# Optimization experiments

Measured on AMD Instinct MI355X. Metric: run time of the kernel, lower is better.

## Reference

```python
import jax, jax.numpy as jnp
import numpy as np

HEADS = 16
DIM_HEAD = 64


def setup_inputs() -> dict:
    key = jax.random.key(0)
    k1, k2, k3, k4 = jax.random.split(key, 4)
    B, T, D = 4, 1024, 1024
    x = jax.random.normal(k1, (B, T, D), dtype=jnp.float32)
    w_qkv = jax.random.normal(k2, (3 * HEADS * DIM_HEAD, D), dtype=jnp.float32) * (1.0 / np.sqrt(D))
    w_out = jax.random.normal(k3, (D, HEADS * DIM_HEAD), dtype=jnp.float32) * (1.0 / np.sqrt(HEADS * DIM_HEAD))
    rel_bias = jax.random.normal(k4, (2 * 1024 - 1, HEADS), dtype=jnp.float32) * 0.02
    return {"x": x, "w_qkv": w_qkv, "w_out": w_out, "rel_bias": rel_bias}


def reference(x, w_qkv, w_out, rel_bias):
    b, t, _ = x.shape
    h, dh = HEADS, DIM_HEAD
    scale = dh ** (-0.5)
    qkv = x @ w_qkv.T  # [b, t, 3*h*dh]
    # einops 'b t (d k h) -> k b h t d': last axis factors as (dh, 3, h)
    qkv = qkv.reshape(b, t, dh, 3, h).transpose(3, 0, 4, 1, 2)  # [3, b, h, t, dh]
    q, k, v = qkv[0], qkv[1], qkv[2]
    scores = jnp.einsum('bhid,bhjd->bhij', q, k) * scale  # [b, h, t, t]
    # relative position bias: rel[i,j] = j - i + t - 1
    rel = jnp.arange(t)[None, :] - jnp.arange(t)[:, None] + (t - 1)  # [t, t]
    bias = rel_bias[rel]  # [t, t, h]
    scores = scores + bias.transpose(2, 0, 1)[None]  # [b, h, t, t]
    attn = jax.nn.softmax(scores, axis=-1)
    out = jnp.einsum('bhij,bhjd->bhid', attn, v)  # [b, h, t, dh]
    out = out.transpose(0, 2, 1, 3).reshape(b, t, h * dh)  # 'b h t d -> b t (h d)'
    return out @ w_out.T
```

## Files before the change

### kernel.cpp

```cpp
#include <hip/hip_runtime.h>
#include <hip/hip_bf16.h>

typedef short bf16x8 __attribute__((ext_vector_type(8)));
typedef float f32x4  __attribute__((ext_vector_type(4)));

typedef __attribute__((address_space(3))) void lds_t;
typedef __attribute__((address_space(1))) void gbl_t;

#define MFMA16(a,b,c) __builtin_amdgcn_mfma_f32_16x16x32_bf16((a),(b),(c),0,0,0)

__device__ __forceinline__ unsigned short f2bf(float f) {
    __hip_bfloat16 h = __float2bfloat16(f);
    return __builtin_bit_cast(unsigned short, h);
}
__device__ __forceinline__ float bf2f(unsigned short u) {
    __hip_bfloat16 h = __builtin_bit_cast(__hip_bfloat16, u);
    return __bfloat162float(h);
}

__global__ void prep_all(const float* __restrict__ x,
                         const float* __restrict__ w_qkv,
                         const float* __restrict__ w_out,
                         unsigned short* __restrict__ A1h,
                         unsigned short* __restrict__ W1h,
                         unsigned short* __restrict__ W3h) {
    const int NX = 4096 * 256, NW1 = 3072 * 256, NW3 = 1024 * 256;
    for (int idx = blockIdx.x * blockDim.x + threadIdx.x; idx < NX + NW1 + NW3;
         idx += gridDim.x * blockDim.x) {
        if (idx < NX) {
            int base = idx * 4;
            float4 v = *reinterpret_cast<const float4*>(x + base);
            ushort4 hi;
            hi.x = f2bf(v.x); hi.y = f2bf(v.y);
            hi.z = f2bf(v.z); hi.w = f2bf(v.w);
            *reinterpret_cast<ushort4*>(A1h + base) = hi;
        } else if (idx < NX + NW1) {
            int base = (idx - NX) * 4;
            int n = base >> 10, c = base & 1023;
            int d = n & 63, which = n >> 10, h = (n >> 6) & 15;
            int srow = d * 48 + which * 16 + h;
            float4 v =
                *reinterpret_cast<const float4*>(w_qkv + (size_t)srow * 1024 + c);
            ushort4 hi;
            hi.x = f2bf(v.x); hi.y = f2bf(v.y);
            hi.z = f2bf(v.z); hi.w = f2bf(v.w);
            *reinterpret_cast<ushort4*>(W1h + (size_t)n * 1024 + c) = hi;
        } else {
            int base = (idx - NX - NW1) * 4;
            float4 v = *reinterpret_cast<const float4*>(w_out + base);
            ushort4 hi;
            hi.x = f2bf(v.x); hi.y = f2bf(v.y);
            hi.z = f2bf(v.z); hi.w = f2bf(v.w);
            *reinterpret_cast<ushort4*>(W3h + base) = hi;
        }
    }
}

__global__ __launch_bounds__(512, 1) void gemm256_hi(
    const unsigned short* __restrict__ A, const unsigned short* __restrict__ B,
    unsigned short* __restrict__ outQ, unsigned short* __restrict__ outK,
    unsigned short* __restrict__ outV) {
    __shared__ unsigned short lds[65536];
    const int tid = threadIdx.x;
    const int wid = tid >> 6, lane = tid & 63;
    const int lrow = lane & 15, lgrp = lane >> 4;
    const int wr = wid >> 2, wc = wid & 3;
    const int mtile = blockIdx.y * 256, ntile = blockIdx.x * 256;

    const int csw0 = (lgrp ^ (lrow & 7)) * 8;
    const int csw1 = ((4 | lgrp) ^ (lrow & 7)) * 8;
    const int arowb = (wr * 128 + lrow) * 64;
    const int browb = (wc * 64 + lrow) * 64;

    const int srow = tid >> 3;
    const int schunk = tid & 7;
    const int gchunk = schunk ^ (srow & 7);
    const unsigned short* Abase = A + (size_t)(mtile + srow) * 1024 + gchunk * 8;
    const unsigned short* Bbase = B + (size_t)(ntile + srow) * 1024 + gchunk * 8;
    const int sdst = srow * 64 + schunk * 8;

    f32x4 acc[8][4];
#pragma unroll
    for (int i = 0; i < 8; ++i)
#pragma unroll
        for (int j = 0; j < 4; ++j) {
            f32x4 z = {0.f, 0.f, 0.f, 0.f};
            acc[i][j] = z;
        }

#pragma unroll
    for (int e = 0; e < 4; ++e)
        __builtin_amdgcn_global_load_lds(
            (const gbl_t*)(Abase + (size_t)e * 64 * 1024),
            (lds_t*)(lds + e * 4096 + sdst), 16, 0, 0);
#pragma unroll
    for (int e = 0; e < 4; ++e)
        __builtin_amdgcn_global_load_lds(
            (const gbl_t*)(Bbase + (size_t)e * 64 * 1024),
            (lds_t*)(lds + 32768 + e * 4096 + sdst), 16, 0, 0);
    asm volatile("s_waitcnt vmcnt(0)" ::: "memory");
    __syncthreads();

    for (int s = 0; s < 16; ++s) {
        const int cur = s & 1;
        const unsigned short* abuf = lds + cur * 16384;
        const unsigned short* bbuf = lds + 32768 + cur * 16384;
        const int nx = cur ^ 1;
        const int kb = (s + 1) * 64;

        if (s < 15) {
#pragma unroll
            for (int e = 0; e < 4; ++e)
                __builtin_amdgcn_global_load_lds(
                    (const gbl_t*)(Abase + (size_t)e * 64 * 1024 + kb),
                    (lds_t*)(lds + nx * 16384 + e * 4096 + sdst), 16, 0, 0);
        }
        {
            bf16x8 af[8], bfv[4];
#pragma unroll
            for (int i = 0; i < 8; ++i)
                af[i] = *reinterpret_cast<const bf16x8*>(abuf + arowb + i * 1024 +
                                                         csw0);
#pragma unroll
            for (int j = 0; j < 4; ++j)
                bfv[j] = *reinterpret_cast<const bf16x8*>(bbuf + browb +
                                                          j * 1024 + csw0);
            __builtin_amdgcn_s_setprio(1);
#pragma unroll
            for (int i = 0; i < 8; ++i)
#pragma unroll
                for (int j = 0; j < 4; ++j)
                    acc[i][j] = MFMA16(af[i], bfv[j], acc[i][j]);
            __builtin_amdgcn_s_setprio(0);
        }
        if (s < 15) {
#pragma unroll
            for (int e = 0; e < 4; ++e)
                __builtin_amdgcn_global_load_lds(
                    (const gbl_t*)(Bbase + (size_t)e * 64 * 1024 + kb),
                    (lds_t*)(lds + 32768 + nx * 16384 + e * 4096 + sdst), 16, 0,
                    0);
        }
        {
            bf16x8 af[8], bfv[4];
#pragma unroll
            for (int i = 0; i < 8; ++i)
                af[i] = *reinterpret_cast<const bf16x8*>(abuf + arowb + i * 1024 +
                                                         csw1);
#pragma unroll
            for (int j = 0; j < 4; ++j)
                bfv[j] = *reinterpret_cast<const bf16x8*>(bbuf + browb +
                                                          j * 1024 + csw1);
            __builtin_amdgcn_s_setprio(1);
#pragma unroll
            for (int i = 0; i < 8; ++i)
#pragma unroll
                for (int j = 0; j < 4; ++j)
                    acc[i][j] = MFMA16(af[i], bfv[j], acc[i][j]);
            __builtin_amdgcn_s_setprio(0);
        }

        if (s < 15) {
            asm volatile("s_waitcnt vmcnt(0)" ::: "memory");
            __syncthreads();
        }
    }

#pragma unroll
    for (int i = 0; i < 8; ++i) {
#pragma unroll
        for (int j = 0; j < 4; ++j) {
#pragma unroll
            for (int r = 0; r < 4; ++r) {
                float v = acc[i][j][r];
                int m = mtile + wr * 128 + i * 16 + lgrp * 4 + r;
                int n = ntile + wc * 64 + j * 16 + lrow;
                int which = n >> 10;
                int hh = (n >> 6) & 15;
                int d = n & 63;
                int b = m >> 10, t = m & 1023;
                unsigned short* dstp =
                    (which == 0) ? outQ : ((which == 1) ? outK : outV);
                dstp[((size_t)((b << 4) + hh) * 1024 + t) * 64 + d] = f2bf(v);
            }
        }
    }
}

__global__ __launch_bounds__(256, 3) void gemm_out_v5(
    const unsigned short* __restrict__ A, const unsigned short* __restrict__ B,
    float* __restrict__ outF) {
    __shared__ unsigned short As[2][64 * 64];
    __shared__ unsigned short Bs[2][128 * 64];
    const int tid = threadIdx.x;
    const int wid = tid >> 6, lane = tid & 63;
    const int lrow = lane & 15, lgrp = lane >> 4;
    const int wr = wid >> 1, wc = wid & 1;
    const int h = blockIdx.x;
    const int xcd = h & 7, within = h >> 3;
    const int mtile = (xcd * 8 + (within & 7)) * 64;
    const int ntile = (within >> 3) * 128;

    const int srow = tid >> 3;
    const int schunk = (tid & 7) ^ (srow & 7);
    const unsigned short* Abase = A + (size_t)(mtile + srow) * 1024 + schunk * 8;
    const unsigned short* Bbase = B + (size_t)(ntile + srow) * 1024 + schunk * 8;

    const int csw0 = (lgrp ^ (lrow & 7)) * 8;
    const int csw1 = ((4 | lgrp) ^ (lrow & 7)) * 8;
    const int arow = wr * 32 + lrow;
    const int brow = wc * 64 + lrow;

    f32x4 acc[2][4];
#pragma unroll
    for (int i = 0; i < 2; ++i)
#pragma unroll
        for (int j = 0; j < 4; ++j) {
            f32x4 z = {0.f, 0.f, 0.f, 0.f};
            acc[i][j] = z;
        }

#pragma unroll
    for (int e = 0; e < 2; ++e)
        __builtin_amdgcn_global_load_lds(
            (const gbl_t*)(Abase + (size_t)e * 32 * 1024),
            (lds_t*)(&As[0][0] + e * 2048 + tid * 8), 16, 0, 0);
#pragma unroll
    for (int e = 0; e < 4; ++e)
        __builtin_amdgcn_global_load_lds(
            (const gbl_t*)(Bbase + (size_t)e * 32 * 1024),
            (lds_t*)(&Bs[0][0] + e * 2048 + tid * 8), 16, 0, 0);
    asm volatile("s_waitcnt vmcnt(0)" ::: "memory");
    __syncthreads();

    for (int s = 0; s < 16; ++s) {
        const int cur = s & 1;
        if (s < 15) {
            const int kb = (s + 1) * 64;
            const int nx = cur ^ 1;
#pragma unroll
            for (int e = 0; e < 2; ++e)
                __builtin_amdgcn_global_load_lds(
                    (const gbl_t*)(Abase + (size_t)e * 32 * 1024 + kb),
                    (lds_t*)(&As[nx][0] + e * 2048 + tid * 8), 16, 0, 0);
#pragma unroll
            for (int e = 0; e < 4; ++e)
                __builtin_amdgcn_global_load_lds(
                    (const gbl_t*)(Bbase + (size_t)e * 32 * 1024 + kb),
                    (lds_t*)(&Bs[nx][0] + e * 2048 + tid * 8), 16, 0, 0);
        }
        bf16x8 a0[2], a1[2], b0[4], b1[4];
#pragma unroll
        for (int i = 0; i < 2; ++i) {
            a0[i] = *reinterpret_cast<const bf16x8*>(&As[cur][0] +
                                                     (arow + i * 16) * 64 + csw0);
            a1[i] = *reinterpret_cast<const bf16x8*>(&As[cur][0] +
                                                     (arow + i * 16) * 64 + csw1);
        }
#pragma unroll
        for (int j = 0; j < 4; ++j) {
            b0[j] = *reinterpret_cast<const bf16x8*>(&Bs[cur][0] +
                                                     (brow + j * 16) * 64 + csw0);
            b1[j] = *reinterpret_cast<const bf16x8*>(&Bs[cur][0] +
                                                     (brow + j * 16) * 64 + csw1);
        }
        __builtin_amdgcn_s_setprio(1);
#pragma unroll
        for (int i = 0; i < 2; ++i)
#pragma unroll
            for (int j = 0; j < 4; ++j) {
                acc[i][j] = MFMA16(a0[i], b0[j], acc[i][j]);
                acc[i][j] = MFMA16(a1[i], b1[j], acc[i][j]);
            }
        __builtin_amdgcn_s_setprio(0);
        if (s < 15) {
            asm volatile("s_waitcnt vmcnt(0)" ::: "memory");
            __syncthreads();
        }
    }

#pragma unroll
    for (int i = 0; i < 2; ++i)
#pragma unroll
        for (int j = 0; j < 4; ++j)
#pragma unroll
            for (int r = 0; r < 4; ++r) {
                int m = mtile + wr * 32 + i * 16 + lgrp * 4 + r;
                int n = ntile + wc * 64 + j * 16 + lrow;
                outF[(size_t)m * 1024 + n] = acc[i][j][r];
            }
}

__global__ __launch_bounds__(256) void transpose_v(
    const unsigned short* __restrict__ Vb, unsigned short* __restrict__ Vtg) {
    __shared__ unsigned short L[64][72];
    const int tt = blockIdx.x, bh = blockIdx.y;
    const int tid = threadIdx.x;
#pragma unroll
    for (int e = 0; e < 2; ++e) {
        int chunk = e * 256 + tid;
        int r = chunk >> 3, c = (chunk & 7) * 8;
        uint4 v = *reinterpret_cast<const uint4*>(
            Vb + ((size_t)bh * 1024 + tt * 64 + r) * 64 + c);
        *reinterpret_cast<uint4*>(&L[r][c]) = v;
    }
    __syncthreads();
#pragma unroll
    for (int e = 0; e < 2; ++e) {
        int chunk = e * 256 + tid;
        int d = chunk >> 3, t0 = (chunk & 7) * 8;
        unsigned short tmp[8];
#pragma unroll
        for (int u = 0; u < 8; ++u) tmp[u] = L[t0 + u][d];
        *reinterpret_cast<uint4*>(Vtg + ((size_t)bh * 64 + d) * 1024 + tt * 64 +
                                  t0) = *reinterpret_cast<const uint4*>(tmp);
    }
}

__global__ __launch_bounds__(512) void attn_kernel(
    const unsigned short* __restrict__ Qb, const unsigned short* __restrict__ Kb,
    const unsigned short* __restrict__ Vtg, const float* __restrict__ rel_bias,
    unsigned short* __restrict__ A3) {
    const int bh = blockIdx.x;
    const int qt = blockIdx.y;
    const int b = bh >> 4, h = bh & 15;
    const int tid = threadIdx.x;
    const int w = tid >> 6, lane = tid & 63;
    const int lrow = lane & 15, lgrp = lane >> 4;
    const float LOG2E = 1.4426950408889634f;
    const float SCALE2 = 0.125f * 1.4426950408889634f;
    const float THR = 11.5f;

    __shared__ unsigned short Ks[2][64 * 64];
    __shared__ unsigned short Vs[2][64 * 64];
    __shared__ unsigned short Ps[8][16 * 64];
    __shared__ float BiasF[1152];

    const unsigned short* Ktile = Kb + (size_t)bh * 1024 * 64;
    const unsigned short* Vtile = Vtg + (size_t)bh * 64 * 1024;

    const unsigned short* Qp =
        Qb + ((size_t)bh * 1024 + qt * 128 + w * 16 + lrow) * 64;
    bf16x8 qa0 = *reinterpret_cast<const bf16x8*>(Qp + lgrp * 8);
    bf16x8 qa1 = *reinterpret_cast<const bf16x8*>(Qp + 32 + lgrp * 8);

    const int sr0 = w * 8 + (lane >> 3);
    const int sc_lo = lane & 7;

    float m_run = -3.0e38f;
    float l_run = 0.f;
    f32x4 o_acc[4];
#pragma unroll
    for (int n = 0; n < 4; n++) {
        f32x4 z = {0.f, 0.f, 0.f, 0.f};
        o_acc[n] = z;
    }

    const int bbase = lgrp * 4 + 127 - w * 16 - lrow;

    {
        {
            int r = sr0;
            int c = sc_lo ^ (r & 7);
            __builtin_amdgcn_global_load_lds(
                (const gbl_t*)(Ktile + (size_t)r * 64 + c * 8),
                (lds_t*)(&Ks[0][0] + w * 512), 16, 0, 0);
            __builtin_amdgcn_global_load_lds(
                (const gbl_t*)(Vtile + (size_t)r * 1024 + c * 8),
                (lds_t*)(&Vs[0][0] + w * 512), 16, 0, 0);
        }
        const int rbase = 896 - qt * 128;
        for (int t = tid; t < 1151; t += 512)
            BiasF[t] = rel_bias[(size_t)(t + rbase) * 16 + h] * LOG2E;
        asm volatile("s_waitcnt vmcnt(0)" ::: "memory");
        __syncthreads();
    }

    for (int kv = 0; kv < 16; ++kv) {
        const int cur = kv & 1;
        const int j0 = kv * 64;
        if (kv < 15) {
            const int j0n = (kv + 1) * 64;
            int r = sr0;
            int c = sc_lo ^ (r & 7);
            __builtin_amdgcn_global_load_lds(
                (const gbl_t*)(Ktile + (size_t)(j0n + r) * 64 + c * 8),
                (lds_t*)(&Ks[cur ^ 1][0] + w * 512), 16, 0, 0);
            __builtin_amdgcn_global_load_lds(
                (const gbl_t*)(Vtile + (size_t)r * 1024 + j0n + c * 8),
                (lds_t*)(&Vs[cur ^ 1][0] + w * 512), 16, 0, 0);
        }

        const unsigned short* kbuf = &Ks[cur][0];
        f32x4 s[4];
        __builtin_amdgcn_s_setprio(1);
#pragma unroll
        for (int f = 0; f < 4; ++f) {
            int krow = f * 16 + lrow;
            int sw0 = (lgrp ^ (lrow & 7)) * 8;
            int sw1 = ((4 | lgrp) ^ (lrow & 7)) * 8;
            bf16x8 kb0 = *reinterpret_cast<const bf16x8*>(kbuf + krow * 64 + sw0);
            bf16x8 kb1 = *reinterpret_cast<const bf16x8*>(kbuf + krow * 64 + sw1);
            f32x4 z = {0.f, 0.f, 0.f, 0.f};
            z = MFMA16(kb0, qa0, z);
            z = MFMA16(kb1, qa1, z);
            s[f] = z;
        }
        __builtin_amdgcn_s_setprio(0);

        float x[4][4];
        float pm = -3.0e38f;
#pragma unroll
        for (int f = 0; f < 4; ++f)
#pragma unroll
            for (int r = 0; r < 4; ++r) {
                float xv = s[f][r] * SCALE2 + BiasF[j0 + bbase + f * 16 + r];
                x[f][r] = xv;
                pm = fmaxf(pm, xv);
            }
        pm = fmaxf(pm, __shfl_xor(pm, 16));
        pm = fmaxf(pm, __shfl_xor(pm, 32));

        if (!__all(pm - m_run <= THR)) {
            float mnew = fmaxf(m_run, pm);
            float corr = __builtin_amdgcn_exp2f(m_run - mnew);
            m_run = mnew;
            l_run *= corr;
            float cb[4];
#pragma unroll
            for (int r = 0; r < 4; ++r) cb[r] = __shfl(corr, lgrp * 4 + r);
#pragma unroll
            for (int n = 0; n < 4; n++)
#pragma unroll
                for (int r = 0; r < 4; r++) o_acc[n][r] *= cb[r];
        }

        float su = 0.f;
#pragma unroll
        for (int f = 0; f < 4; ++f)
#pragma unroll
            for (int r = 0; r < 4; ++r) {
                float pv = __builtin_amdgcn_exp2f(x[f][r] - m_run);
                x[f][r] = pv;
                su += pv;
            }
        l_run += su;

#pragma unroll
        for (int f = 0; f < 4; ++f) {
            unsigned int plo, phi;
            asm("v_cvt_pk_bf16_f32 %0, %1, %2"
                : "=v"(plo)
                : "v"(x[f][0]), "v"(x[f][1]));
            asm("v_cvt_pk_bf16_f32 %0, %1, %2"
                : "=v"(phi)
                : "v"(x[f][2]), "v"(x[f][3]));
            const int chunk = (f * 2 + (lgrp >> 1)) ^ (lrow & 7);
            uint2 pw;
            pw.x = plo;
            pw.y = phi;
            *reinterpret_cast<uint2*>(
                &Ps[w][lrow * 64 + chunk * 8 + (lgrp & 1) * 4]) = pw;
        }

        const unsigned short* vbuf = &Vs[cur][0];
        __builtin_amdgcn_s_setprio(1);
#pragma unroll
        for (int jc = 0; jc < 2; ++jc) {
            int pc = ((4 * jc + lgrp) ^ (lrow & 7)) * 8;
            bf16x8 pa =
                *reinterpret_cast<const bf16x8*>(&Ps[w][0] + lrow * 64 + pc);
#pragma unroll
            for (int n = 0; n < 4; n++) {
                int vrow = n * 16 + lrow;
                bf16x8 vb =
                    *reinterpret_cast<const bf16x8*>(vbuf + vrow * 64 + pc);
                o_acc[n] = MFMA16(pa, vb, o_acc[n]);
            }
        }
        __builtin_amdgcn_s_setprio(0);

        if (kv < 15) {
            asm volatile("s_waitcnt vmcnt(0)" ::: "memory");
            __syncthreads();
        }
    }

    float lt = l_run + __shfl_xor(l_run, 16);
    lt += __shfl_xor(lt, 32);
    float rl[4];
#pragma unroll
    for (int r = 0; r < 4; ++r) rl[r] = 1.0f / __shfl(lt, lgrp * 4 + r);

#pragma unroll
    for (int n = 0; n < 4; n++) {
#pragma unroll
        for (int r = 0; r < 4; r++) {
            float val = o_acc[n][r] * rl[r];
            int ia = qt * 128 + w * 16 + lgrp * 4 + r;
            size_t m = (size_t)b * 1024 + ia;
            int col = h * 64 + n * 16 + lrow;
            A3[m * 1024 + col] = f2bf(val);
        }
    }
}

extern "C" void kernel_launch(void* const* d_in, const int* in_sizes, int n_in,
                              void* d_out, int out_size, void* d_ws,
                              size_t ws_size, hipStream_t stream) {
    const float* x = (const float*)d_in[0];
    const float* w_qkv = (const float*)d_in[1];
    const float* w_out = (const float*)d_in[2];
    const float* rel_bias = (const float*)d_in[3];
    float* out = (float*)d_out;

    char* ws = (char*)d_ws;
    size_t off = 0;
    auto alloc = [&](size_t bytes) {
        char* p = ws + off;
        off += (bytes + 255) & ~(size_t)255;
        return p;
    };
    unsigned short* A1h = (unsigned short*)alloc((size_t)4096 * 1024 * 2);
    unsigned short* W1h = (unsigned short*)alloc((size_t)3072 * 1024 * 2);
    unsigned short* Qb = (unsigned short*)alloc((size_t)64 * 1024 * 64 * 2);
    unsigned short* Kb = (unsigned short*)alloc((size_t)64 * 1024 * 64 * 2);
    unsigned short* Vb = (unsigned short*)alloc((size_t)64 * 1024 * 64 * 2);
    unsigned short* A3h = (unsigned short*)alloc((size_t)4096 * 1024 * 2);
    unsigned short* W3h = (unsigned short*)alloc((size_t)1024 * 1024 * 2);
    unsigned short* Vtg = A1h;

    hipLaunchKernelGGL(prep_all, dim3(2048), dim3(256), 0, stream, x, w_qkv,
                       w_out, A1h, W1h, W3h);
    hipLaunchKernelGGL(gemm256_hi, dim3(12, 16), dim3(512), 0, stream, A1h, W1h,
                       Qb, Kb, Vb);
    hipLaunchKernelGGL(transpose_v, dim3(16, 64), dim3(256), 0, stream, Vb, Vtg);
    hipLaunchKernelGGL(attn_kernel, dim3(64, 8), dim3(512), 0, stream, Qb, Kb,
                       Vtg, rel_bias, A3h);
    hipLaunchKernelGGL(gemm_out_v5, dim3(512), dim3(256), 0, stream, A3h, W3h,
                       out);
}
```

Baseline: 97.94 us.

## Process two query sub-tiles per attention block to reuse K/V tiles

Each attention workgroup now handles 256 query rows, as two 128-row halves per wave, instead of 128, and the grid is halved to 64x4. Each K/V tile staged in LDS is reused for twice as many queries, which halves global K/V traffic and the number of block barriers per query. In exchange the kernel holds more registers for two sets of accumulators and softmax state, uses more LDS, and launches only 256 blocks, which may leave compute units idle on a 256-CU part.

After: 103.9 us. +6.1%, slower.

```diff
diff --git a/kernel.cpp b/kernel.cpp
--- a/kernel.cpp
+++ b/kernel.cpp
@@ -333,30 +333,36 @@
 
     __shared__ unsigned short Ks[2][64 * 64];
     __shared__ unsigned short Vs[2][64 * 64];
-    __shared__ unsigned short Ps[8][16 * 64];
-    __shared__ float BiasF[1152];
+    __shared__ unsigned short Ps[8][2 * 1024];
+    __shared__ float BiasF[1280];
 
     const unsigned short* Ktile = Kb + (size_t)bh * 1024 * 64;
     const unsigned short* Vtile = Vtg + (size_t)bh * 64 * 1024;
 
-    const unsigned short* Qp =
-        Qb + ((size_t)bh * 1024 + qt * 128 + w * 16 + lrow) * 64;
-    bf16x8 qa0 = *reinterpret_cast<const bf16x8*>(Qp + lgrp * 8);
-    bf16x8 qa1 = *reinterpret_cast<const bf16x8*>(Qp + 32 + lgrp * 8);
+    bf16x8 qa[2][2];
+#pragma unroll
+    for (int ih = 0; ih < 2; ++ih) {
+        const unsigned short* Qp =
+            Qb + ((size_t)bh * 1024 + qt * 256 + ih * 128 + w * 16 + lrow) * 64;
+        qa[ih][0] = *reinterpret_cast<const bf16x8*>(Qp + lgrp * 8);
+        qa[ih][1] = *reinterpret_cast<const bf16x8*>(Qp + 32 + lgrp * 8);
+    }
 
     const int sr0 = w * 8 + (lane >> 3);
     const int sc_lo = lane & 7;
 
-    float m_run = -3.0e38f;
-    float l_run = 0.f;
-    f32x4 o_acc[4];
-#pragma unroll
-    for (int n = 0; n < 4; n++) {
-        f32x4 z = {0.f, 0.f, 0.f, 0.f};
-        o_acc[n] = z;
-    }
-
-    const int bbase = lgrp * 4 + 127 - w * 16 - lrow;
+    float m_run[2] = {-3.0e38f, -3.0e38f};
+    float l_run[2] = {0.f, 0.f};
+    f32x4 o_acc[2][4];
+#pragma unroll
+    for (int ih = 0; ih < 2; ++ih)
+#pragma unroll
+        for (int n = 0; n < 4; n++) {
+            f32x4 z = {0.f, 0.f, 0.f, 0.f};
+            o_acc[ih][n] = z;
+        }
+
+    const int bbase0 = lgrp * 4 + 255 - w * 16 - lrow;
 
     {
         {
@@ -369,8 +375,8 @@
                 (const gbl_t*)(Vtile + (size_t)r * 1024 + c * 8),
                 (lds_t*)(&Vs[0][0] + w * 512), 16, 0, 0);
         }
-        const int rbase = 896 - qt * 128;
-        for (int t = tid; t < 1151; t += 512)
+        const int rbase = 768 - qt * 256;
+        for (int t = tid; t < 1279; t += 512)
             BiasF[t] = rel_bias[(size_t)(t + rbase) * 16 + h] * LOG2E;
         asm volatile("s_waitcnt vmcnt(0)" ::: "memory");
         __syncthreads();
@@ -392,93 +398,101 @@
         }
 
         const unsigned short* kbuf = &Ks[cur][0];
-        f32x4 s[4];
-        __builtin_amdgcn_s_setprio(1);
-#pragma unroll
-        for (int f = 0; f < 4; ++f) {
-            int krow = f * 16 + lrow;
-            int sw0 = (lgrp ^ (lrow & 7)) * 8;
-            int sw1 = ((4 | lgrp) ^ (lrow & 7)) * 8;
-            bf16x8 kb0 = *reinterpret_cast<const bf16x8*>(kbuf + krow * 64 + sw0);
-            bf16x8 kb1 = *reinterpret_cast<const bf16x8*>(kbuf + krow * 64 + sw1);
-            f32x4 z = {0.f, 0.f, 0.f, 0.f};
-            z = MFMA16(kb0, qa0, z);
-            z = MFMA16(kb1, qa1, z);
-            s[f] = z;
-        }
-        __builtin_amdgcn_s_setprio(0);
-
-        float x[4][4];
-        float pm = -3.0e38f;
-#pragma unroll
-        for (int f = 0; f < 4; ++f)
-#pragma unroll
-            for (int r = 0; r < 4; ++r) {
-                float xv = s[f][r] * SCALE2 + BiasF[j0 + bbase + f * 16 + r];
-                x[f][r] = xv;
-                pm = fmaxf(pm, xv);
-            }
-        pm = fmaxf(pm, __shfl_xor(pm, 16));
-        pm = fmaxf(pm, __shfl_xor(pm, 32));
-
-        if (!__all(pm - m_run <= THR)) {
-            float mnew = fmaxf(m_run, pm);
-            float corr = __builtin_amdgcn_exp2f(m_run - mnew);
-            m_run = mnew;
-            l_run *= corr;
-            float cb[4];
-#pragma unroll
-            for (int r = 0; r < 4; ++r) cb[r] = __shfl(corr, lgrp * 4 + r);
-#pragma unroll
-            for (int n = 0; n < 4; n++)
-#pragma unroll
-                for (int r = 0; r < 4; r++) o_acc[n][r] *= cb[r];
-        }
-
-        float su = 0.f;
-#pragma unroll
-        for (int f = 0; f < 4; ++f)
-#pragma unroll
-            for (int r = 0; r < 4; ++r) {
-                float pv = __builtin_amdgcn_exp2f(x[f][r] - m_run);
-                x[f][r] = pv;
-                su += pv;
-            }
-        l_run += su;
-
-#pragma unroll
-        for (int f = 0; f < 4; ++f) {
-            unsigned int plo, phi;
-            asm("v_cvt_pk_bf16_f32 %0, %1, %2"
-                : "=v"(plo)
-                : "v"(x[f][0]), "v"(x[f][1]));
-            asm("v_cvt_pk_bf16_f32 %0, %1, %2"
-                : "=v"(phi)
-                : "v"(x[f][2]), "v"(x[f][3]));
-            const int chunk = (f * 2 + (lgrp >> 1)) ^ (lrow & 7);
-            uint2 pw;
-            pw.x = plo;
-            pw.y = phi;
-            *reinterpret_cast<uint2*>(
-                &Ps[w][lrow * 64 + chunk * 8 + (lgrp & 1) * 4]) = pw;
-        }
-
         const unsigned short* vbuf = &Vs[cur][0];
-        __builtin_amdgcn_s_setprio(1);
-#pragma unroll
-        for (int jc = 0; jc < 2; ++jc) {
-            int pc = ((4 * jc + lgrp) ^ (lrow & 7)) * 8;
-            bf16x8 pa =
-                *reinterpret_cast<const bf16x8*>(&Ps[w][0] + lrow * 64 + pc);
-#pragma unroll
-            for (int n = 0; n < 4; n++) {
-                int vrow = n * 16 + lrow;
-                bf16x8 vb =
-                    *reinterpret_cast<const bf16x8*>(vbuf + vrow * 64 + pc);
-                o_acc[n] = MFMA16(pa, vb, o_acc[n]);
-            }
-        }
-        __builtin_amdgcn_s_setprio(0);
+
+#pragma unroll
+        for (int ih = 0; ih < 2; ++ih) {
+            f32x4 s[4];
+            __builtin_amdgcn_s_setprio(1);
+#pragma unroll
+            for (int f = 0; f < 4; ++f) {
+                int krow = f * 16 + lrow;
+                int sw0 = (lgrp ^ (lrow & 7)) * 8;
+                int sw1 = ((4 | lgrp) ^ (lrow & 7)) * 8;
+                bf16x8 kb0 =
+                    *reinterpret_cast<const bf16x8*>(kbuf + krow * 64 + sw0);
+                bf16x8 kb1 =
+                    *reinterpret_cast<const bf16x8*>(kbuf + krow * 64 + sw1);
+                f32x4 z = {0.f, 0.f, 0.f, 0.f};
+                z = MFMA16(kb0, qa[ih][0], z);
+                z = MFMA16(kb1, qa[ih][1], z);
+                s[f] = z;
+            }
+            __builtin_amdgcn_s_setprio(0);
+
+            const int bb = j0 + bbase0 - ih * 128;
+            float x[4][4];
+            float pm = -3.0e38f;
+#pragma unroll
+            for (int f = 0; f < 4; ++f)
+#pragma unroll
+                for (int r = 0; r < 4; ++r) {
+                    float xv = s[f][r] * SCALE2 + BiasF[bb + f * 16 + r];
+                    x[f][r] = xv;
+                    pm = fmaxf(pm, xv);
+                }
+            pm = fmaxf(pm, __shfl_xor(pm, 16));
+            pm = fmaxf(pm, __shfl_xor(pm, 32));
+
+            if (!__all(pm - m_run[ih] <= THR)) {
+                float mnew = fmaxf(m_run[ih], pm);
+                float corr = __builtin_amdgcn_exp2f(m_run[ih] - mnew);
+                m_run[ih] = mnew;
+                l_run[ih] *= corr;
+                float cb[4];
+#pragma unroll
+                for (int r = 0; r < 4; ++r) cb[r] = __shfl(corr, lgrp * 4 + r);
+#pragma unroll
+                for (int n = 0; n < 4; n++)
+#pragma unroll
+                    for (int r = 0; r < 4; r++) o_acc[ih][n][r] *= cb[r];
+            }
+
+            float su = 0.f;
+#pragma unroll
+            for (int f = 0; f < 4; ++f)
+#pragma unroll
+                for (int r = 0; r < 4; ++r) {
+                    float pv = __builtin_amdgcn_exp2f(x[f][r] - m_run[ih]);
+                    x[f][r] = pv;
+                    su += pv;
+                }
+            l_run[ih] += su;
+
+            unsigned short* psec = &Ps[w][ih * 1024];
+#pragma unroll
+            for (int f = 0; f < 4; ++f) {
+                unsigned int plo, phi;
+                asm("v_cvt_pk_bf16_f32 %0, %1, %2"
+                    : "=v"(plo)
+                    : "v"(x[f][0]), "v"(x[f][1]));
+                asm("v_cvt_pk_bf16_f32 %0, %1, %2"
+                    : "=v"(phi)
+                    : "v"(x[f][2]), "v"(x[f][3]));
+                const int chunk = (f * 2 + (lgrp >> 1)) ^ (lrow & 7);
+                uint2 pw;
+                pw.x = plo;
+                pw.y = phi;
+                *reinterpret_cast<uint2*>(
+                    &psec[lrow * 64 + chunk * 8 + (lgrp & 1) * 4]) = pw;
+            }
+
+            __builtin_amdgcn_s_setprio(1);
+#pragma unroll
+            for (int jc = 0; jc < 2; ++jc) {
+                int pc = ((4 * jc + lgrp) ^ (lrow & 7)) * 8;
+                bf16x8 pa =
+                    *reinterpret_cast<const bf16x8*>(psec + lrow * 64 + pc);
+#pragma unroll
+                for (int n = 0; n < 4; n++) {
+                    int vrow = n * 16 + lrow;
+                    bf16x8 vb =
+                        *reinterpret_cast<const bf16x8*>(vbuf + vrow * 64 + pc);
+                    o_acc[ih][n] = MFMA16(pa, vb, o_acc[ih][n]);
+                }
+            }
+            __builtin_amdgcn_s_setprio(0);
+        }
 
         if (kv < 15) {
             asm volatile("s_waitcnt vmcnt(0)" ::: "memory");
@@ -486,21 +500,23 @@
         }
     }
 
-    float lt = l_run + __shfl_xor(l_run, 16);
-    lt += __shfl_xor(lt, 32);
-    float rl[4];
-#pragma unroll
-    for (int r = 0; r < 4; ++r) rl[r] = 1.0f / __shfl(lt, lgrp * 4 + r);
-
-#pragma unroll
-    for (int n = 0; n < 4; n++) {
-#pragma unroll
-        for (int r = 0; r < 4; r++) {
-            float val = o_acc[n][r] * rl[r];
-            int ia = qt * 128 + w * 16 + lgrp * 4 + r;
-            size_t m = (size_t)b * 1024 + ia;
-            int col = h * 64 + n * 16 + lrow;
-            A3[m * 1024 + col] = f2bf(val);
+#pragma unroll
+    for (int ih = 0; ih < 2; ++ih) {
+        float lt = l_run[ih] + __shfl_xor(l_run[ih], 16);
+        lt += __shfl_xor(lt, 32);
+        float rl[4];
+#pragma unroll
+        for (int r = 0; r < 4; ++r) rl[r] = 1.0f / __shfl(lt, lgrp * 4 + r);
+#pragma unroll
+        for (int n = 0; n < 4; n++) {
+#pragma unroll
+            for (int r = 0; r < 4; r++) {
+                float val = o_acc[ih][n][r] * rl[r];
+                int ia = qt * 256 + ih * 128 + w * 16 + lgrp * 4 + r;
+                size_t m = (size_t)b * 1024 + ia;
+                int col = h * 64 + n * 16 + lrow;
+                A3[m * 1024 + col] = f2bf(val);
+            }
         }
     }
 }
@@ -535,7 +551,7 @@
     hipLaunchKernelGGL(gemm256_hi, dim3(12, 16), dim3(512), 0, stream, A1h, W1h,
                        Qb, Kb, Vb);
     hipLaunchKernelGGL(transpose_v, dim3(16, 64), dim3(256), 0, stream, Vb, Vtg);
-    hipLaunchKernelGGL(attn_kernel, dim3(64, 8), dim3(512), 0, stream, Qb, Kb,
+    hipLaunchKernelGGL(attn_kernel, dim3(64, 4), dim3(512), 0, stream, Qb, Kb,
                        Vtg, rel_bias, A3h);
     hipLaunchKernelGGL(gemm_out_v5, dim3(512), dim3(256), 0, stream, A3h, W3h,
                        out);
```
